# Kernel optimization log

Hardware: AMD Instinct MI355X
Metric: run time of the kernel (lower is better)

Reference implementation:

```python
import jax, jax.numpy as jnp
import numpy as np

EMBED_DIM = 1024
NUM_HEADS = 16
HEAD_DIM = EMBED_DIM // NUM_HEADS
ROPE_BASE = 10000.0


def setup_inputs() -> dict:
    key = jax.random.key(0)
    ks = jax.random.split(key, 12)
    B, T, M, D = 4, 2048, 2048, EMBED_DIM
    query = jax.random.normal(ks[0], (B, T, D), dtype=jnp.float32)
    k_in = jax.random.normal(ks[1], (B, M, D), dtype=jnp.float32)
    v_in = jax.random.normal(ks[2], (B, M, D), dtype=jnp.float32)
    query_position_ids = jnp.sort(
        jax.random.randint(ks[3], (B, T), 0, 4096), axis=-1
    ).astype(jnp.int64)
    # xavier-uniform-ish projection weights, zero biases (as in _reset_parameters)
    lim = float(np.sqrt(6.0 / (D + D)))
    Wq = jax.random.uniform(ks[4], (D, D), minval=-lim, maxval=lim, dtype=jnp.float32)
    Wk = jax.random.uniform(ks[5], (D, D), minval=-lim, maxval=lim, dtype=jnp.float32)
    Wv = jax.random.uniform(ks[6], (D, D), minval=-lim, maxval=lim, dtype=jnp.float32)
    Wo = jax.random.uniform(ks[7], (D, D), minval=-lim, maxval=lim, dtype=jnp.float32)
    bq = jnp.zeros((D,), jnp.float32)
    bk = jnp.zeros((D,), jnp.float32)
    bv = jnp.zeros((D,), jnp.float32)
    bo = jnp.zeros((D,), jnp.float32)
    return dict(query=query, key=k_in, value=v_in,
                query_position_ids=query_position_ids,
                Wq=Wq, bq=bq, Wk=Wk, bk=bk, Wv=Wv, bv=bv, Wo=Wo, bo=bo)


def _apply_rope(q, position_ids):
    # q: [B, T, H, hd]; position_ids: [B, T]
    hd = q.shape[-1]
    inv_freq = 1.0 / (ROPE_BASE ** (jnp.arange(0, hd, 2, dtype=jnp.float32) / hd))
    ang = position_ids.astype(jnp.float32)[:, :, None] * inv_freq  # [B, T, hd/2]
    cos = jnp.cos(ang)[:, :, None, :]  # [B, T, 1, hd/2]
    sin = jnp.sin(ang)[:, :, None, :]
    q1, q2 = q[..., : hd // 2], q[..., hd // 2:]
    return jnp.concatenate([q1 * cos - q2 * sin, q2 * cos + q1 * sin], axis=-1)


def reference(query, key, value, query_position_ids, Wq, bq, Wk, bk, Wv, bv, Wo, bo):
    B, T, D = query.shape
    M = key.shape[1]
    H, hd = NUM_HEADS, HEAD_DIM
    scaling = 1.0 / np.sqrt(hd)
    q = (query @ Wq.T + bq).reshape(B, T, H, hd)
    k = (key @ Wk.T + bk).reshape(B, M, H, hd)
    v = (value @ Wv.T + bv).reshape(B, M, H, hd)
    q = _apply_rope(q, query_position_ids)
    # scores: [B, H, T, M]
    scores = jnp.einsum('bthd,bmhd->bhtm', q, k) * scaling
    attn = jax.nn.softmax(scores, axis=-1)
    out = jnp.einsum('bhtm,bmhd->bthd', attn, v).reshape(B, T, D)
    return out @ Wo.T + bo
```

## Files before the change

kernel.cpp:

```cpp
#include <hip/hip_runtime.h>
#include <hip/hip_bf16.h>
#include <math.h>

typedef __hip_bfloat16 bf16;
typedef __attribute__((ext_vector_type(8))) short bf16x8;
typedef __attribute__((ext_vector_type(4))) float f32x4;

#define D_MODEL 1024
#define N_HEADS 16
#define HEAD_D  64
#define SEQ     2048
#define BATCH   4
#define NROWS   (BATCH*SEQ)

#define SCALE_Q 0.18033688011112042f

#define MFMA(a,b,c) __builtin_amdgcn_mfma_f32_16x16x32_bf16(a,b,c,0,0,0)

#if __has_builtin(__builtin_amdgcn_exp2f)
#define EXP2(x) __builtin_amdgcn_exp2f(x)
#else
#define EXP2(x) exp2f(x)
#endif

__device__ __forceinline__ void gload16(void* lds_uniform_base, const void* g) {
  __builtin_amdgcn_global_load_lds(
      (const __attribute__((address_space(1))) void*)g,
      (__attribute__((address_space(3))) void*)lds_uniform_base,
      16, 0, 0);
}

__device__ __forceinline__ unsigned pkrne(float a, float b) {
  unsigned ua = __float_as_uint(a), ub = __float_as_uint(b);
  ua += 0x7FFFu + ((ua >> 16) & 1u);
  ub += 0x7FFFu + ((ub >> 16) & 1u);
  return (ua >> 16) | (ub & 0xFFFF0000u);
}
__device__ __forceinline__ bf16x8 cvt8rne(float4 a, float4 b) {
  union { bf16x8 v; unsigned u[4]; } u;
  u.u[0] = pkrne(a.x, a.y); u.u[1] = pkrne(a.z, a.w);
  u.u[2] = pkrne(b.x, b.y); u.u[3] = pkrne(b.z, b.w);
  return u.v;
}

__global__ __launch_bounds__(256)
void convw(const float* __restrict__ src, bf16* __restrict__ dst) {
  int idx = (blockIdx.x * 256 + threadIdx.x) * 8;
  float4 a = *(const float4*)(src + idx);
  float4 b = *(const float4*)(src + idx + 4);
  *(bf16x8*)(dst + idx) = cvt8rne(a, b);
}

template<int MODE, bool A_BF16, bool B_BF16>
__global__ __launch_bounds__(256, 2)
void gemm_bt(const void* __restrict__ Xv, const void* __restrict__ Wv,
             const float* __restrict__ bias, void* __restrict__ outv,
             const int* __restrict__ pos) {
  __shared__ bf16 sA[128*64];
  __shared__ bf16 sB[128*64];

  const float* Xf = (const float*)Xv;
  const bf16*  Xb = (const bf16*) Xv;
  const float* Wf = (const float*)Wv;
  const bf16*  Wb = (const bf16*) Wv;

  const int tid  = threadIdx.x;
  const int lane = tid & 63, wid = tid >> 6;
  const int q4 = lane >> 4, l15 = lane & 15;
  const int rb = blockIdx.x * 128;
  const int cb = blockIdx.y * 128;
  const int wm = (wid >> 1) * 64, wn = (wid & 1) * 64;

  f32x4 acc[4][4];
  const f32x4 z4 = {0.f, 0.f, 0.f, 0.f};
#pragma unroll
  for (int i = 0; i < 4; ++i)
#pragma unroll
    for (int j = 0; j < 4; ++j) acc[i][j] = z4;

  for (int kt = 0; kt < 16; ++kt) {
    const int k0 = kt * 64;
    if (A_BF16) {
#pragma unroll
      for (int i = 0; i < 4; ++i) {
        int o  = i*4096 + tid*16;
        int rr = o >> 7;
        int c0 = ((o >> 4) & 7) ^ (rr & 7);
        gload16((char*)sA + i*4096 + (wid << 10),
                Xb + (size_t)(rb + rr)*D_MODEL + k0 + c0*8);
      }
    }
    if (B_BF16) {
#pragma unroll
      for (int i = 0; i < 4; ++i) {
        int o  = i*4096 + tid*16;
        int rr = o >> 7;
        int c0 = ((o >> 4) & 7) ^ (rr & 7);
        gload16((char*)sB + i*4096 + (wid << 10),
                Wb + (size_t)(cb + rr)*D_MODEL + k0 + c0*8);
      }
    }
    if (!A_BF16) {
#pragma unroll
      for (int i = 0; i < 4; ++i) {
        int e  = i*2048 + tid*8;
        int rr = e >> 6, c = (e >> 3) & 7, cs = c ^ (rr & 7);
        const float* s0 = Xf + (size_t)(rb + rr)*D_MODEL + k0 + c*8;
        *(bf16x8*)((char*)sA + rr*128 + cs*16) =
            cvt8rne(*(const float4*)s0, *(const float4*)(s0 + 4));
      }
    }
    if (!B_BF16) {
#pragma unroll
      for (int i = 0; i < 4; ++i) {
        int e  = i*2048 + tid*8;
        int rr = e >> 6, c = (e >> 3) & 7, cs = c ^ (rr & 7);
        const float* s1 = Wf + (size_t)(cb + rr)*D_MODEL + k0 + c*8;
        *(bf16x8*)((char*)sB + rr*128 + cs*16) =
            cvt8rne(*(const float4*)s1, *(const float4*)(s1 + 4));
      }
    }
    __syncthreads();
#pragma unroll
    for (int kq = 0; kq < 2; ++kq) {
      bf16x8 af[4], bfr[4];
      const int cc = (kq*4 + q4) ^ (l15 & 7);
#pragma unroll
      for (int mi = 0; mi < 4; ++mi) {
        int r = wm + mi*16 + l15;
        af[mi] = *(const bf16x8*)((const char*)sA + r*128 + cc*16);
      }
#pragma unroll
      for (int ni = 0; ni < 4; ++ni) {
        int r = wn + ni*16 + l15;
        bfr[ni] = *(const bf16x8*)((const char*)sB + r*128 + cc*16);
      }
#pragma unroll
      for (int mi = 0; mi < 4; ++mi)
#pragma unroll
        for (int ni = 0; ni < 4; ++ni)
          acc[mi][ni] = MFMA(af[mi], bfr[ni], acc[mi][ni]);
    }
    __syncthreads();
  }

  if (MODE == 0) {
    float* outF = (float*)outv;
#pragma unroll
    for (int ni = 0; ni < 4; ++ni) {
      int col = cb + wn + ni*16 + l15;
      float bv = bias[col];
#pragma unroll
      for (int mi = 0; mi < 4; ++mi) {
        int row0 = rb + wm + mi*16 + q4*4;
#pragma unroll
        for (int r = 0; r < 4; ++r)
          outF[(size_t)(row0 + r)*D_MODEL + col] = acc[mi][ni][r] + bv;
      }
    }
  } else if (MODE == 1) {
    bf16* out = (bf16*)outv;
#pragma unroll
    for (int ni = 0; ni < 4; ++ni) {
      int col = cb + wn + ni*16 + l15;
      int h = col >> 6, d = col & 63;
      float bv = bias[col];
#pragma unroll
      for (int mi = 0; mi < 4; ++mi) {
#pragma unroll
        for (int r = 0; r < 4; ++r) {
          int row = rb + wm + mi*16 + q4*4 + r;
          int b = row >> 11, m = row & 2047;
          out[(size_t)((b*N_HEADS + h)*SEQ + m)*HEAD_D + d] =
              __float2bfloat16(acc[mi][ni][r] + bv);
        }
      }
    }
  } else if (MODE == 2) {
    bf16* out = (bf16*)outv;
#pragma unroll
    for (int mi = 0; mi < 4; ++mi) {
#pragma unroll
      for (int r = 0; r < 4; ++r) {
        int row = rb + wm + mi*16 + q4*4 + r;
        float bv = bias[row];
#pragma unroll
        for (int ni = 0; ni < 4; ++ni) {
          int col = cb + wn + ni*16 + l15;
          int b = col >> 11, m = col & 2047;
          out[(size_t)(b*D_MODEL + row)*SEQ + m] =
              __float2bfloat16(acc[mi][ni][r] + bv);
        }
      }
    }
  } else {
    bf16* out = (bf16*)outv;
    const bool is64 = (pos[NROWS - 1] == 0);
    const float CLOG = 13.287712379549449f / 32.0f;
    float invf0 = exp2f(-(float)(l15)      * CLOG);
    float invf1 = exp2f(-(float)(l15 + 16) * CLOG);
    int h = (cb + wn) >> 6;
#pragma unroll
    for (int ni = 0; ni < 2; ++ni) {
      int col1 = cb + wn + ni*16 + l15;
      int d = ni*16 + l15;
      float invf = (ni == 0) ? invf0 : invf1;
      float b1 = bias[col1];
      float b2 = bias[col1 + 32];
#pragma unroll
      for (int mi = 0; mi < 4; ++mi) {
#pragma unroll
        for (int r = 0; r < 4; ++r) {
          int row = rb + wm + mi*16 + q4*4 + r;
          int b = row >> 11, t = row & 2047;
          int pv = is64 ? pos[2*row] : pos[row];
          float ang = (float)pv * invf;
          float sn, cs;
          __sincosf(ang, &sn, &cs);
          float q1 = acc[mi][ni][r]   + b1;
          float q2 = acc[mi][ni+2][r] + b2;
          size_t base = (size_t)((b*N_HEADS + h)*SEQ + t)*HEAD_D;
          out[base + d]      = __float2bfloat16((q1*cs - q2*sn) * SCALE_Q);
          out[base + d + 32] = __float2bfloat16((q2*cs + q1*sn) * SCALE_Q);
        }
      }
    }
  }
}

__global__ __launch_bounds__(256, 2)
void attn_kernel(const bf16* __restrict__ Q, const bf16* __restrict__ K,
                 const bf16* __restrict__ VT, bf16* __restrict__ O) {
  __shared__ __align__(16) char smem[34816 + 16384];
  bf16* sP  = (bf16*)smem;
  bf16* sK  = (bf16*)smem;
  bf16* sVT = (bf16*)(smem + 34816);

  const int tid  = threadIdx.x;
  const int lane = tid & 63, wid = tid >> 6;
  const int q4 = lane >> 4, l15 = lane & 15;
  const int bh = blockIdx.y;
  const int qb = blockIdx.x * 128;

  const bf16* Qp  = Q  + (size_t)bh * SEQ * HEAD_D;
  const bf16* Kp  = K  + (size_t)bh * SEQ * HEAD_D;
  const bf16* VTp = VT + (size_t)bh * HEAD_D * SEQ;

  bf16x8 qf[2][2];
#pragma unroll
  for (int mi = 0; mi < 2; ++mi)
#pragma unroll
    for (int kq = 0; kq < 2; ++kq) {
      int t = qb + wid*32 + mi*16 + l15;
      qf[mi][kq] = *(const bf16x8*)(Qp + (size_t)t*HEAD_D + kq*32 + q4*8);
    }

  const f32x4 z4 = {0.f, 0.f, 0.f, 0.f};
  f32x4 oacc[2][4];
  float mrow[2][4], lrow[2][4];
#pragma unroll
  for (int mi = 0; mi < 2; ++mi) {
#pragma unroll
    for (int nd = 0; nd < 4; ++nd) oacc[mi][nd] = z4;
#pragma unroll
    for (int r = 0; r < 4; ++r) { mrow[mi][r] = -3.0e38f; lrow[mi][r] = 0.f; }
  }

  for (int kv = 0; kv < 16; ++kv) {
    const int m0 = kv * 128;
#pragma unroll
    for (int i = 0; i < 4; ++i) {
      int o  = i*4096 + tid*16;
      int rr = o >> 7;
      int c0 = ((o >> 4) & 7) ^ (rr & 7);
      gload16((char*)sK + i*4096 + (wid << 10),
              Kp + (size_t)(m0 + rr)*HEAD_D + c0*8);
    }
#pragma unroll
    for (int i = 0; i < 4; ++i) {
      int o  = i*4096 + tid*16;
      int rr = o >> 8;
      int c0 = ((o >> 4) & 15) ^ (rr & 7);
      gload16((char*)sVT + i*4096 + (wid << 10),
              VTp + (size_t)rr*SEQ + m0 + c0*8);
    }
    __syncthreads();

    f32x4 s[2][8];
#pragma unroll
    for (int mi = 0; mi < 2; ++mi)
#pragma unroll
      for (int ni = 0; ni < 8; ++ni) s[mi][ni] = z4;
#pragma unroll
    for (int kq = 0; kq < 2; ++kq) {
      const int cc = (kq*4 + q4) ^ (l15 & 7);
#pragma unroll
      for (int ni = 0; ni < 8; ++ni) {
        int m = ni*16 + l15;
        bf16x8 bk = *(const bf16x8*)((const char*)sK + m*128 + cc*16);
        s[0][ni] = MFMA(qf[0][kq], bk, s[0][ni]);
        s[1][ni] = MFMA(qf[1][kq], bk, s[1][ni]);
      }
    }
    __syncthreads();

#pragma unroll
    for (int mi = 0; mi < 2; ++mi) {
      float mloc[4] = {-3.0e38f, -3.0e38f, -3.0e38f, -3.0e38f};
#pragma unroll
      for (int ni = 0; ni < 8; ++ni)
#pragma unroll
        for (int r = 0; r < 4; ++r) mloc[r] = fmaxf(mloc[r], s[mi][ni][r]);
#pragma unroll
      for (int off = 1; off < 16; off <<= 1)
#pragma unroll
        for (int r = 0; r < 4; ++r)
          mloc[r] = fmaxf(mloc[r], __shfl_xor(mloc[r], off, 64));
      float al[4], rs[4] = {0.f, 0.f, 0.f, 0.f};
#pragma unroll
      for (int r = 0; r < 4; ++r) {
        float mn = fmaxf(mrow[mi][r], mloc[r]);
        al[r] = EXP2(mrow[mi][r] - mn);
        mrow[mi][r] = mn;
      }
#pragma unroll
      for (int ni = 0; ni < 8; ++ni)
#pragma unroll
        for (int r = 0; r < 4; ++r) {
          float p = EXP2(s[mi][ni][r] - mrow[mi][r]);
          s[mi][ni][r] = p;
          rs[r] += p;
        }
#pragma unroll
      for (int r = 0; r < 4; ++r) lrow[mi][r] = lrow[mi][r]*al[r] + rs[r];
#pragma unroll
      for (int nd = 0; nd < 4; ++nd)
#pragma unroll
        for (int r = 0; r < 4; ++r) oacc[mi][nd][r] *= al[r];
#pragma unroll
      for (int ni = 0; ni < 8; ++ni)
#pragma unroll
        for (int r = 0; r < 4; ++r)
          sP[(wid*32 + mi*16 + q4*4 + r)*136 + ni*16 + l15] =
              __float2bfloat16(s[mi][ni][r]);
    }
    __syncthreads();

#pragma unroll
    for (int kk = 0; kk < 4; ++kk) {
      bf16x8 bv[4];
      const int cc = (kk*4 + q4) ^ (l15 & 7);
#pragma unroll
      for (int nd = 0; nd < 4; ++nd) {
        int d = nd*16 + l15;
        bv[nd] = *(const bf16x8*)((const char*)sVT + d*256 + cc*16);
      }
#pragma unroll
      for (int mi = 0; mi < 2; ++mi) {
        bf16x8 ap = *(const bf16x8*)((const char*)sP +
                     (wid*32 + mi*16 + l15)*272 + kk*64 + q4*16);
#pragma unroll
        for (int nd = 0; nd < 4; ++nd)
          oacc[mi][nd] = MFMA(ap, bv[nd], oacc[mi][nd]);
      }
    }
    __syncthreads();
  }

  const int b = bh >> 4, h = bh & 15;
#pragma unroll
  for (int mi = 0; mi < 2; ++mi) {
#pragma unroll
    for (int r = 0; r < 4; ++r) {
      float l = lrow[mi][r];
      l += __shfl_xor(l, 1, 64);
      l += __shfl_xor(l, 2, 64);
      l += __shfl_xor(l, 4, 64);
      l += __shfl_xor(l, 8, 64);
      float inv = 1.0f / l;
      int t = qb + wid*32 + mi*16 + q4*4 + r;
#pragma unroll
      for (int nd = 0; nd < 4; ++nd) {
        int d = nd*16 + l15;
        O[(size_t)(b*SEQ + t)*D_MODEL + h*HEAD_D + d] =
            __float2bfloat16(oacc[mi][nd][r] * inv);
      }
    }
  }
}

extern "C" void kernel_launch(void* const* d_in, const int* in_sizes, int n_in,
                              void* d_out, int out_size, void* d_ws, size_t ws_size,
                              hipStream_t stream) {
  const void* query = d_in[0];
  const void* key   = d_in[1];
  const void* value = d_in[2];
  const int*  pos   = (const int*)d_in[3];
  const float* Wq = (const float*)d_in[4];  const float* bq = (const float*)d_in[5];
  const float* Wk = (const float*)d_in[6];  const float* bk = (const float*)d_in[7];
  const float* Wv = (const float*)d_in[8];  const float* bv = (const float*)d_in[9];
  const float* Wo = (const float*)d_in[10]; const float* bo = (const float*)d_in[11];

  char* ws = (char*)d_ws;
  bf16* qbuf  = (bf16*)(ws);
  bf16* kbuf  = (bf16*)(ws + (size_t)16777216);
  bf16* vtbuf = (bf16*)(ws + (size_t)33554432);
  bf16* obuf  = (bf16*)(ws + (size_t)50331648);
  bf16* wqb = obuf;
  bf16* wkb = obuf + (size_t)1048576;
  bf16* wvb = obuf + (size_t)2097152;

  dim3 blk(256);
  dim3 gproj(NROWS/128, D_MODEL/128);
  dim3 gprojT(D_MODEL/128, NROWS/128);

  convw<<<512, blk, 0, stream>>>(Wq, wqb);
  convw<<<512, blk, 0, stream>>>(Wk, wkb);
  convw<<<512, blk, 0, stream>>>(Wv, wvb);

  gemm_bt<3, false, true ><<<gproj,  blk, 0, stream>>>(query, wqb, bq, qbuf, pos);
  gemm_bt<1, false, true ><<<gproj,  blk, 0, stream>>>(key,   wkb, bk, kbuf, nullptr);
  gemm_bt<2, true,  false><<<gprojT, blk, 0, stream>>>(wvb, value, bv, vtbuf, nullptr);

  attn_kernel<<<dim3(SEQ/128, BATCH*N_HEADS), blk, 0, stream>>>(qbuf, kbuf, vtbuf, obuf);

  gemm_bt<0, true,  false><<<gproj,  blk, 0, stream>>>(obuf, Wo, bo, d_out, nullptr);
  (void)in_sizes; (void)n_in; (void)out_size; (void)ws_size;
}
```

Measured before the change: 442.9 us.

## Pre-convert activations to bf16 and rework attention to register-resident K/V loads

Activations (value, key, query) and Wo are converted to bf16 in separate passes, with d_out and qbuf used as scratch, so every GEMM can stage both operands through async 16-byte global-to-LDS loads instead of converting fp32 inline. The attention kernel no longer stages K and V^T in shared memory. It reads them directly from global into registers, computes transposed score tiles (K as the A operand) so each row's softmax needs only two cross-lane shuffles, and keeps a per-wave P buffer so all block barriers are dropped. The cost is extra conversion launches and round trips through global memory, plus uncoalesced, possibly L2-dependent K/V reads inside the attention loop.

```diff
diff --git a/kernel.cpp b/kernel.cpp
--- a/kernel.cpp
+++ b/kernel.cpp
@@ -51,18 +51,13 @@
   *(bf16x8*)(dst + idx) = cvt8rne(a, b);
 }
 
-template<int MODE, bool A_BF16, bool B_BF16>
+template<int MODE>
 __global__ __launch_bounds__(256, 2)
-void gemm_bt(const void* __restrict__ Xv, const void* __restrict__ Wv,
+void gemm_bt(const bf16* __restrict__ Xb, const bf16* __restrict__ Wb,
              const float* __restrict__ bias, void* __restrict__ outv,
              const int* __restrict__ pos) {
   __shared__ bf16 sA[128*64];
   __shared__ bf16 sB[128*64];
-
-  const float* Xf = (const float*)Xv;
-  const bf16*  Xb = (const bf16*) Xv;
-  const float* Wf = (const float*)Wv;
-  const bf16*  Wb = (const bf16*) Wv;
 
   const int tid  = threadIdx.x;
   const int lane = tid & 63, wid = tid >> 6;
@@ -80,45 +75,15 @@
 
   for (int kt = 0; kt < 16; ++kt) {
     const int k0 = kt * 64;
-    if (A_BF16) {
-#pragma unroll
-      for (int i = 0; i < 4; ++i) {
-        int o  = i*4096 + tid*16;
-        int rr = o >> 7;
-        int c0 = ((o >> 4) & 7) ^ (rr & 7);
-        gload16((char*)sA + i*4096 + (wid << 10),
-                Xb + (size_t)(rb + rr)*D_MODEL + k0 + c0*8);
-      }
-    }
-    if (B_BF16) {
-#pragma unroll
-      for (int i = 0; i < 4; ++i) {
-        int o  = i*4096 + tid*16;
-        int rr = o >> 7;
-        int c0 = ((o >> 4) & 7) ^ (rr & 7);
-        gload16((char*)sB + i*4096 + (wid << 10),
-                Wb + (size_t)(cb + rr)*D_MODEL + k0 + c0*8);
-      }
-    }
-    if (!A_BF16) {
-#pragma unroll
-      for (int i = 0; i < 4; ++i) {
-        int e  = i*2048 + tid*8;
-        int rr = e >> 6, c = (e >> 3) & 7, cs = c ^ (rr & 7);
-        const float* s0 = Xf + (size_t)(rb + rr)*D_MODEL + k0 + c*8;
-        *(bf16x8*)((char*)sA + rr*128 + cs*16) =
-            cvt8rne(*(const float4*)s0, *(const float4*)(s0 + 4));
-      }
-    }
-    if (!B_BF16) {
-#pragma unroll
-      for (int i = 0; i < 4; ++i) {
-        int e  = i*2048 + tid*8;
-        int rr = e >> 6, c = (e >> 3) & 7, cs = c ^ (rr & 7);
-        const float* s1 = Wf + (size_t)(cb + rr)*D_MODEL + k0 + c*8;
-        *(bf16x8*)((char*)sB + rr*128 + cs*16) =
-            cvt8rne(*(const float4*)s1, *(const float4*)(s1 + 4));
-      }
+#pragma unroll
+    for (int i = 0; i < 4; ++i) {
+      int o  = i*4096 + tid*16;
+      int rr = o >> 7;
+      int c0 = ((o >> 4) & 7) ^ (rr & 7);
+      gload16((char*)sA + i*4096 + (wid << 10),
+              Xb + (size_t)(rb + rr)*D_MODEL + k0 + c0*8);
+      gload16((char*)sB + i*4096 + (wid << 10),
+              Wb + (size_t)(cb + rr)*D_MODEL + k0 + c0*8);
     }
     __syncthreads();
 #pragma unroll
@@ -231,10 +196,7 @@
 __global__ __launch_bounds__(256, 2)
 void attn_kernel(const bf16* __restrict__ Q, const bf16* __restrict__ K,
                  const bf16* __restrict__ VT, bf16* __restrict__ O) {
-  __shared__ __align__(16) char smem[34816 + 16384];
-  bf16* sP  = (bf16*)smem;
-  bf16* sK  = (bf16*)smem;
-  bf16* sVT = (bf16*)(smem + 34816);
+  __shared__ __align__(16) bf16 sP[4 * 32 * 128];
 
   const int tid  = threadIdx.x;
   const int lane = tid & 63, wid = tid >> 6;
@@ -245,6 +207,7 @@
   const bf16* Qp  = Q  + (size_t)bh * SEQ * HEAD_D;
   const bf16* Kp  = K  + (size_t)bh * SEQ * HEAD_D;
   const bf16* VTp = VT + (size_t)bh * HEAD_D * SEQ;
+  char* wP = (char*)sP + wid * 8192;
 
   bf16x8 qf[2][2];
 #pragma unroll
@@ -257,134 +220,104 @@
 
   const f32x4 z4 = {0.f, 0.f, 0.f, 0.f};
   f32x4 oacc[2][4];
-  float mrow[2][4], lrow[2][4];
+  float mrow[2], lrow[2];
 #pragma unroll
   for (int mi = 0; mi < 2; ++mi) {
 #pragma unroll
     for (int nd = 0; nd < 4; ++nd) oacc[mi][nd] = z4;
-#pragma unroll
-    for (int r = 0; r < 4; ++r) { mrow[mi][r] = -3.0e38f; lrow[mi][r] = 0.f; }
+    mrow[mi] = -3.0e38f; lrow[mi] = 0.f;
   }
 
   for (int kv = 0; kv < 16; ++kv) {
     const int m0 = kv * 128;
-#pragma unroll
-    for (int i = 0; i < 4; ++i) {
-      int o  = i*4096 + tid*16;
-      int rr = o >> 7;
-      int c0 = ((o >> 4) & 7) ^ (rr & 7);
-      gload16((char*)sK + i*4096 + (wid << 10),
-              Kp + (size_t)(m0 + rr)*HEAD_D + c0*8);
-    }
-#pragma unroll
-    for (int i = 0; i < 4; ++i) {
-      int o  = i*4096 + tid*16;
-      int rr = o >> 8;
-      int c0 = ((o >> 4) & 15) ^ (rr & 7);
-      gload16((char*)sVT + i*4096 + (wid << 10),
-              VTp + (size_t)rr*SEQ + m0 + c0*8);
-    }
-    __syncthreads();
-
-    f32x4 s[2][8];
+
+    f32x4 st[2][8];
 #pragma unroll
     for (int mi = 0; mi < 2; ++mi)
 #pragma unroll
-      for (int ni = 0; ni < 8; ++ni) s[mi][ni] = z4;
+      for (int ni = 0; ni < 8; ++ni) st[mi][ni] = z4;
 #pragma unroll
     for (int kq = 0; kq < 2; ++kq) {
-      const int cc = (kq*4 + q4) ^ (l15 & 7);
 #pragma unroll
       for (int ni = 0; ni < 8; ++ni) {
-        int m = ni*16 + l15;
-        bf16x8 bk = *(const bf16x8*)((const char*)sK + m*128 + cc*16);
-        s[0][ni] = MFMA(qf[0][kq], bk, s[0][ni]);
-        s[1][ni] = MFMA(qf[1][kq], bk, s[1][ni]);
-      }
-    }
-    __syncthreads();
+        bf16x8 kf = *(const bf16x8*)(Kp + (size_t)(m0 + ni*16 + l15)*HEAD_D
+                                        + kq*32 + q4*8);
+        st[0][ni] = MFMA(kf, qf[0][kq], st[0][ni]);
+        st[1][ni] = MFMA(kf, qf[1][kq], st[1][ni]);
+      }
+    }
 
 #pragma unroll
     for (int mi = 0; mi < 2; ++mi) {
-      float mloc[4] = {-3.0e38f, -3.0e38f, -3.0e38f, -3.0e38f};
+      float mloc = st[mi][0][0];
 #pragma unroll
       for (int ni = 0; ni < 8; ++ni)
 #pragma unroll
-        for (int r = 0; r < 4; ++r) mloc[r] = fmaxf(mloc[r], s[mi][ni][r]);
-#pragma unroll
-      for (int off = 1; off < 16; off <<= 1)
-#pragma unroll
-        for (int r = 0; r < 4; ++r)
-          mloc[r] = fmaxf(mloc[r], __shfl_xor(mloc[r], off, 64));
-      float al[4], rs[4] = {0.f, 0.f, 0.f, 0.f};
-#pragma unroll
-      for (int r = 0; r < 4; ++r) {
-        float mn = fmaxf(mrow[mi][r], mloc[r]);
-        al[r] = EXP2(mrow[mi][r] - mn);
-        mrow[mi][r] = mn;
-      }
+        for (int r = 0; r < 4; ++r) mloc = fmaxf(mloc, st[mi][ni][r]);
+      mloc = fmaxf(mloc, __shfl_xor(mloc, 16, 64));
+      mloc = fmaxf(mloc, __shfl_xor(mloc, 32, 64));
+      float mn = fmaxf(mrow[mi], mloc);
+      float al = EXP2(mrow[mi] - mn);
+      mrow[mi] = mn;
+      float rs = 0.f;
 #pragma unroll
       for (int ni = 0; ni < 8; ++ni)
 #pragma unroll
         for (int r = 0; r < 4; ++r) {
-          float p = EXP2(s[mi][ni][r] - mrow[mi][r]);
-          s[mi][ni][r] = p;
-          rs[r] += p;
+          float p = EXP2(st[mi][ni][r] - mn);
+          st[mi][ni][r] = p;
+          rs += p;
         }
-#pragma unroll
-      for (int r = 0; r < 4; ++r) lrow[mi][r] = lrow[mi][r]*al[r] + rs[r];
+      lrow[mi] = lrow[mi]*al + rs;
 #pragma unroll
       for (int nd = 0; nd < 4; ++nd)
 #pragma unroll
-        for (int r = 0; r < 4; ++r) oacc[mi][nd][r] *= al[r];
-#pragma unroll
-      for (int ni = 0; ni < 8; ++ni)
-#pragma unroll
-        for (int r = 0; r < 4; ++r)
-          sP[(wid*32 + mi*16 + q4*4 + r)*136 + ni*16 + l15] =
-              __float2bfloat16(s[mi][ni][r]);
-    }
-    __syncthreads();
+        for (int r = 0; r < 4; ++r) oacc[mi][nd][r] *= al;
+      char* rowp = wP + (mi*16 + l15)*256;
+#pragma unroll
+      for (int ni = 0; ni < 8; ++ni) {
+        uint2 pk;
+        pk.x = pkrne(st[mi][ni][0], st[mi][ni][1]);
+        pk.y = pkrne(st[mi][ni][2], st[mi][ni][3]);
+        int c  = 2*ni + (q4 >> 1);
+        int cs = c ^ (l15 & 7);
+        *(uint2*)(rowp + cs*16 + 8*(q4 & 1)) = pk;
+      }
+    }
 
 #pragma unroll
     for (int kk = 0; kk < 4; ++kk) {
-      bf16x8 bv[4];
-      const int cc = (kk*4 + q4) ^ (l15 & 7);
-#pragma unroll
-      for (int nd = 0; nd < 4; ++nd) {
-        int d = nd*16 + l15;
-        bv[nd] = *(const bf16x8*)((const char*)sVT + d*256 + cc*16);
-      }
+      bf16x8 vf[4];
+#pragma unroll
+      for (int nd = 0; nd < 4; ++nd)
+        vf[nd] = *(const bf16x8*)(VTp + (size_t)(nd*16 + l15)*SEQ
+                                      + m0 + kk*32 + q4*8);
 #pragma unroll
       for (int mi = 0; mi < 2; ++mi) {
-        bf16x8 ap = *(const bf16x8*)((const char*)sP +
-                     (wid*32 + mi*16 + l15)*272 + kk*64 + q4*16);
+        int cs = (4*kk + q4) ^ (l15 & 7);
+        bf16x8 pb = *(const bf16x8*)(wP + (mi*16 + l15)*256 + cs*16);
 #pragma unroll
         for (int nd = 0; nd < 4; ++nd)
-          oacc[mi][nd] = MFMA(ap, bv[nd], oacc[mi][nd]);
-      }
-    }
-    __syncthreads();
+          oacc[mi][nd] = MFMA(vf[nd], pb, oacc[mi][nd]);
+      }
+    }
   }
 
   const int b = bh >> 4, h = bh & 15;
 #pragma unroll
   for (int mi = 0; mi < 2; ++mi) {
-#pragma unroll
-    for (int r = 0; r < 4; ++r) {
-      float l = lrow[mi][r];
-      l += __shfl_xor(l, 1, 64);
-      l += __shfl_xor(l, 2, 64);
-      l += __shfl_xor(l, 4, 64);
-      l += __shfl_xor(l, 8, 64);
-      float inv = 1.0f / l;
-      int t = qb + wid*32 + mi*16 + q4*4 + r;
-#pragma unroll
-      for (int nd = 0; nd < 4; ++nd) {
-        int d = nd*16 + l15;
-        O[(size_t)(b*SEQ + t)*D_MODEL + h*HEAD_D + d] =
-            __float2bfloat16(oacc[mi][nd][r] * inv);
-      }
+    float l = lrow[mi];
+    l += __shfl_xor(l, 16, 64);
+    l += __shfl_xor(l, 32, 64);
+    float inv = 1.0f / l;
+    int t = qb + wid*32 + mi*16 + l15;
+#pragma unroll
+    for (int nd = 0; nd < 4; ++nd) {
+      uint2 pk;
+      pk.x = pkrne(oacc[mi][nd][0]*inv, oacc[mi][nd][1]*inv);
+      pk.y = pkrne(oacc[mi][nd][2]*inv, oacc[mi][nd][3]*inv);
+      int d = nd*16 + 4*q4;
+      *(uint2*)(O + (size_t)(b*SEQ + t)*D_MODEL + h*HEAD_D + d) = pk;
     }
   }
 }
@@ -392,10 +325,10 @@
 extern "C" void kernel_launch(void* const* d_in, const int* in_sizes, int n_in,
                               void* d_out, int out_size, void* d_ws, size_t ws_size,
                               hipStream_t stream) {
-  const void* query = d_in[0];
-  const void* key   = d_in[1];
-  const void* value = d_in[2];
-  const int*  pos   = (const int*)d_in[3];
+  const float* query = (const float*)d_in[0];
+  const float* key   = (const float*)d_in[1];
+  const float* value = (const float*)d_in[2];
+  const int*   pos   = (const int*)d_in[3];
   const float* Wq = (const float*)d_in[4];  const float* bq = (const float*)d_in[5];
   const float* Wk = (const float*)d_in[6];  const float* bk = (const float*)d_in[7];
   const float* Wv = (const float*)d_in[8];  const float* bv = (const float*)d_in[9];
@@ -409,6 +342,8 @@
   bf16* wqb = obuf;
   bf16* wkb = obuf + (size_t)1048576;
   bf16* wvb = obuf + (size_t)2097152;
+  bf16* wob = qbuf;
+  bf16* xact = (bf16*)d_out;
 
   dim3 blk(256);
   dim3 gproj(NROWS/128, D_MODEL/128);
@@ -418,12 +353,18 @@
   convw<<<512, blk, 0, stream>>>(Wk, wkb);
   convw<<<512, blk, 0, stream>>>(Wv, wvb);
 
-  gemm_bt<3, false, true ><<<gproj,  blk, 0, stream>>>(query, wqb, bq, qbuf, pos);
-  gemm_bt<1, false, true ><<<gproj,  blk, 0, stream>>>(key,   wkb, bk, kbuf, nullptr);
-  gemm_bt<2, true,  false><<<gprojT, blk, 0, stream>>>(wvb, value, bv, vtbuf, nullptr);
+  convw<<<4096, blk, 0, stream>>>(value, xact);
+  gemm_bt<2><<<gprojT, blk, 0, stream>>>(wvb, xact, bv, vtbuf, nullptr);
+
+  convw<<<4096, blk, 0, stream>>>(key, xact);
+  gemm_bt<1><<<gproj,  blk, 0, stream>>>(xact, wkb, bk, kbuf, nullptr);
+
+  convw<<<4096, blk, 0, stream>>>(query, xact);
+  gemm_bt<3><<<gproj,  blk, 0, stream>>>(xact, wqb, bq, qbuf, pos);
 
   attn_kernel<<<dim3(SEQ/128, BATCH*N_HEADS), blk, 0, stream>>>(qbuf, kbuf, vtbuf, obuf);
 
-  gemm_bt<0, true,  false><<<gproj,  blk, 0, stream>>>(obuf, Wo, bo, d_out, nullptr);
+  convw<<<512, blk, 0, stream>>>(Wo, wob);
+  gemm_bt<0><<<gproj,  blk, 0, stream>>>(obuf, wob, bo, d_out, nullptr);
   (void)in_sizes; (void)n_in; (void)out_size; (void)ws_size;
 }
```

Measured after the change: 516.5 us. 1.17x slower.
